# Performance work log

Hardware: AMD Instinct MI355X
Metric: run time of the kernel (lower is better)

## Reference

```python
import jax, jax.numpy as jnp
import numpy as np

C = 256
INTER = C // 8  # 32

def setup_inputs() -> dict:
    key = jax.random.key(0)
    ks = jax.random.split(key, 7)
    B, H, W = 8, 64, 64
    x = jax.random.normal(ks[0], (B, C, H, W), dtype=jnp.float32)
    # 1x1 convs == per-pixel linear maps
    Wq = jax.random.normal(ks[1], (INTER, C), dtype=jnp.float32) * (1.0 / np.sqrt(C))
    bq = jnp.zeros((INTER,), dtype=jnp.float32)
    Wk = jax.random.normal(ks[2], (INTER, C), dtype=jnp.float32) * (1.0 / np.sqrt(C))
    bk = jnp.zeros((INTER,), dtype=jnp.float32)
    Wv = jax.random.normal(ks[3], (C, C), dtype=jnp.float32) * (1.0 / np.sqrt(C))
    bv = jnp.zeros((C,), dtype=jnp.float32)
    gamma = jnp.asarray([0.1], dtype=jnp.float32)  # nonzero so attention path matters
    return {"x": x, "Wq": Wq, "bq": bq, "Wk": Wk, "bk": bk, "Wv": Wv, "bv": bv, "gamma": gamma}

def reference(x, Wq, bq, Wk, bk, Wv, bv, gamma):
    B, Cc, H, W = x.shape
    N = H * W
    xf = x.reshape(B, Cc, N)  # [B, C, N]
    # 1x1 conv projections (per-pixel linear)
    q = jnp.einsum('ic,bcn->bni', Wq, xf) + bq[None, None, :]   # [B, N, inter]
    k = jnp.einsum('ic,bcn->bin', Wk, xf) + bk[None, :, None]   # [B, inter, N]
    v = jnp.einsum('oc,bcn->bon', Wv, xf) + bv[None, :, None]   # [B, C, N]
    energy = jnp.einsum('bni,bim->bnm', q, k)                   # [B, N, N], unscaled
    attn = jax.nn.softmax(energy, axis=-1)                      # softmax over keys
    # out[b,c,i] = sum_j v[b,c,j] * attn[b,i,j]
    out = jnp.einsum('bcj,bij->bci', v, attn).reshape(B, Cc, H, W)
    return gamma[0] * out + x
```

## Files before the change

kernel.cpp:

```cpp
#include <hip/hip_runtime.h>
#include <hip/hip_bf16.h>

#define CCH 256
#define NPIX 4096
#define NB 8
#define LOG2E 1.4426950408889634f

typedef __attribute__((ext_vector_type(8))) short bf16x8;
typedef __attribute__((ext_vector_type(16))) float f32x16;

typedef __attribute__((address_space(3))) unsigned lds_u32;
typedef const __attribute__((address_space(1))) unsigned glb_u32;
#define GL_LDS16(gp, lp) \
    __builtin_amdgcn_global_load_lds((glb_u32*)(gp), (lds_u32*)(lp), 16, 0, 0)

static __device__ __forceinline__ unsigned pkbf(float a, float b) {
    union { __hip_bfloat16 h[2]; unsigned u; } p;
    p.h[0] = __float2bfloat16(a);
    p.h[1] = __float2bfloat16(b);
    return p.u;
}
static __device__ __forceinline__ unsigned short bf1(float a) {
    union { __hip_bfloat16 h; unsigned short s; } p;
    p.h = __float2bfloat16(a);
    return p.s;
}

__global__ void packw_kernel(const float* __restrict__ Wq,
                             const float* __restrict__ Wk,
                             const float* __restrict__ Wv,
                             unsigned short* __restrict__ Wb) {
    int i4 = blockIdx.x * 256 + threadIdx.x;
    if (i4 >= 20480) return;
    int e = i4 * 4;
    const float* src;
    if (e < 8192)       src = Wq + e;
    else if (e < 16384) src = Wk + (e - 8192);
    else                src = Wv + (e - 16384);
    float4 v = *(const float4*)src;
    uint2 o;
    o.x = pkbf(v.x, v.y);
    o.y = pkbf(v.z, v.w);
    *(uint2*)(Wb + e) = o;
}

__global__ __launch_bounds__(320) void qkv_kernel(
    const float* __restrict__ x,
    const unsigned short* __restrict__ Wb,
    const float* __restrict__ bq, const float* __restrict__ bk,
    const float* __restrict__ bv,
    unsigned short* __restrict__ q, unsigned short* __restrict__ k,
    unsigned short* __restrict__ v)
{
    __shared__ __align__(16) unsigned xp[128][36];

    const int t   = threadIdx.x;
    const int b   = blockIdx.x >> 7;
    const int px0 = (blockIdx.x & 127) * 32;

    const float4* gx = (const float4*)x + ((size_t)b * CCH * NPIX + px0) / 4;
    for (int i = t; i < 1024; i += 320) {
        int kp = i >> 3, p4 = i & 7;
        float4 lo = gx[(size_t)(2 * kp) * (NPIX / 4) + p4];
        float4 hi = gx[(size_t)(2 * kp + 1) * (NPIX / 4) + p4];
        uint4 pk4;
        pk4.x = pkbf(lo.x, hi.x);
        pk4.y = pkbf(lo.y, hi.y);
        pk4.z = pkbf(lo.z, hi.z);
        pk4.w = pkbf(lo.w, hi.w);
        *(uint4*)&xp[kp][p4 * 4] = pk4;
    }
    __syncthreads();

    const int w  = t >> 6;
    const int lane = t & 63;
    const int qi = lane & 31, h = lane >> 5;

    f32x16 acc[2];
    #pragma unroll
    for (int rt = 0; rt < 2; ++rt)
        #pragma unroll
        for (int r = 0; r < 16; ++r) acc[rt][r] = 0.f;

    #pragma unroll 4
    for (int ks = 0; ks < 16; ++ks) {
        union { unsigned uw[4]; bf16x8 v8; } xb;
        #pragma unroll
        for (int j = 0; j < 4; ++j) xb.uw[j] = xp[ks * 8 + 4 * h + j][qi];
        #pragma unroll
        for (int rt = 0; rt < 2; ++rt) {
            int row = (2 * w + rt) * 32 + qi;
            bf16x8 af = *(const bf16x8*)(Wb + (size_t)row * 256 + ks * 16 + h * 8);
            acc[rt] = __builtin_amdgcn_mfma_f32_32x32x16_bf16(af, xb.v8, acc[rt], 0, 0, 0);
        }
    }

    const int px = px0 + qi;
    const int pxv = px0 + ((qi & 19) | ((qi & 4) << 1) | ((qi & 8) >> 1));
    #pragma unroll
    for (int rt = 0; rt < 2; ++rt) {
        int tile = 2 * w + rt;
        if (tile < 2) {
            const float* bias = (tile == 0) ? bq : bk;
            unsigned short* outp = (tile == 0) ? q : k;
            float scale = (tile == 0) ? LOG2E : 1.0f;
            #pragma unroll
            for (int rg = 0; rg < 4; ++rg) {
                float vv[4];
                #pragma unroll
                for (int j = 0; j < 4; ++j) {
                    int outd = j + 8 * rg + 4 * h;
                    vv[j] = (acc[rt][4 * rg + j] + bias[outd]) * scale;
                }
                uint2 st;
                st.x = pkbf(vv[0], vv[1]);
                st.y = pkbf(vv[2], vv[3]);
                *(uint2*)(outp + ((size_t)b * NPIX + px) * 32 + 8 * rg + 4 * h) = st;
            }
        } else {
            #pragma unroll
            for (int r = 0; r < 16; ++r) {
                int outd = (r & 3) + 8 * (r >> 2) + 4 * h;
                int grow = (tile - 2) * 32 + outd;
                v[((size_t)b * CCH + grow) * NPIX + pxv] = bf1(acc[rt][r] + bv[grow]);
            }
        }
    }
}

__global__ __launch_bounds__(256, 2) void attn_kernel(
    const unsigned short* __restrict__ qg,
    const unsigned short* __restrict__ kg,
    const unsigned short* __restrict__ vg,
    const float* __restrict__ x,
    const float* __restrict__ gamma,
    float* __restrict__ out)
{
    __shared__ __align__(16) unsigned short Kl[3][64][4][8];
    __shared__ __align__(16) unsigned short Vl[3][128][8][8];

    const int t    = threadIdx.x;
    const int b    = blockIdx.x & 7;
    const int nc   = blockIdx.x >> 3;
    const int chh  = nc & 1;
    const int n0   = (nc >> 1) * 128;
    const int w    = t >> 6;
    const int lane = t & 63;
    const int qi = lane & 31, h = lane >> 5;

    bf16x8 qf0, qf1;
    {
        const unsigned short* qp = qg + ((size_t)b * NPIX + n0 + w * 32 + qi) * 32;
        qf0 = *(const bf16x8*)(qp + h * 8);
        qf1 = *(const bf16x8*)(qp + 16 + h * 8);
    }

    f32x16 acc[4];
    #pragma unroll
    for (int ct = 0; ct < 4; ++ct)
        #pragma unroll
        for (int r = 0; r < 16; ++r) acc[ct][r] = 0.f;
    float l_run = 0.f;

    const int srow = t >> 2;
    const unsigned short* kg_src =
        kg + ((size_t)b * NPIX + srow) * 32 + ((t & 3) ^ (srow & 3)) * 8;
    const int vrow = t >> 3;
    const unsigned short* vg_src =
        vg + ((size_t)b * CCH + chh * 128 + vrow) * NPIX + ((t & 7) ^ (vrow & 7)) * 8;
    char* kl_dst = (char*)Kl + t * 16;
    char* vl_dst = (char*)Vl + t * 16;

    const unsigned short* krd[2][2];
    #pragma unroll
    for (int sub = 0; sub < 2; ++sub)
        #pragma unroll
        for (int s = 0; s < 2; ++s)
            krd[sub][s] = &Kl[0][sub * 32 + qi][(2 * s + h) ^ (qi & 3)][0];
    const unsigned short* vrd[4];
    #pragma unroll
    for (int s = 0; s < 4; ++s)
        vrd[s] = &Vl[0][qi][(2 * s + h) ^ (qi & 7)][0];

    auto STAGE = [&](int buf, int kt) {
        const int k0 = kt * 64;
        GL_LDS16(kg_src + (size_t)k0 * 32, kl_dst + buf * 4096);
        #pragma unroll
        for (int p = 0; p < 4; ++p)
            GL_LDS16(vg_src + k0 + (size_t)p * 32 * NPIX,
                     vl_dst + buf * 16384 + p * 4096);
    };

    auto QKSM = [&](int kb, bf16x8* pf) {
        f32x16 s0, s1;
        #pragma unroll
        for (int r = 0; r < 16; ++r) { s0[r] = 0.f; s1[r] = 0.f; }
        s0 = __builtin_amdgcn_mfma_f32_32x32x16_bf16(*(const bf16x8*)(krd[0][0] + kb * 2048), qf0, s0, 0, 0, 0);
        s0 = __builtin_amdgcn_mfma_f32_32x32x16_bf16(*(const bf16x8*)(krd[0][1] + kb * 2048), qf1, s0, 0, 0, 0);
        s1 = __builtin_amdgcn_mfma_f32_32x32x16_bf16(*(const bf16x8*)(krd[1][0] + kb * 2048), qf0, s1, 0, 0, 0);
        s1 = __builtin_amdgcn_mfma_f32_32x32x16_bf16(*(const bf16x8*)(krd[1][1] + kb * 2048), qf1, s1, 0, 0, 0);
        #pragma unroll
        for (int sub = 0; sub < 2; ++sub) {
            const f32x16& sv = sub ? s1 : s0;
            #pragma unroll
            for (int sp = 0; sp < 2; ++sp) {
                union { unsigned uw[4]; bf16x8 v8; } pk;
                float ps = 0.f;
                #pragma unroll
                for (int c = 0; c < 4; ++c) {
                    float ea = exp2f(sv[8 * sp + 2 * c]);
                    float eb = exp2f(sv[8 * sp + 2 * c + 1]);
                    ps += ea + eb;
                    pk.uw[c] = pkbf(ea, eb);
                }
                l_run += ps;
                pf[2 * sub + sp] = pk.v8;
            }
        }
    };

    auto PV = [&](int vb, const bf16x8* pf) {
        __builtin_amdgcn_s_setprio(1);
        #pragma unroll
        for (int ct = 0; ct < 4; ++ct) {
            #pragma unroll
            for (int s = 0; s < 4; ++s) {
                bf16x8 vf = *(const bf16x8*)(vrd[s] + vb * 8192 + ct * 2048);
                acc[ct] = __builtin_amdgcn_mfma_f32_32x32x16_bf16(vf, pf[s], acc[ct], 0, 0, 0);
            }
        }
        __builtin_amdgcn_s_setprio(0);
    };

#define VMBAR(N) do { asm volatile("s_waitcnt vmcnt(" #N ")" ::: "memory"); \
                      __builtin_amdgcn_s_barrier(); } while (0)

    bf16x8 pfA[4], pfB[4], pfC[4];

    STAGE(0, 0);
    VMBAR(0);
    STAGE(1, 1);
    QKSM(0, pfA);
    VMBAR(4);

    #pragma unroll 1
    for (int m = 0; m < 20; ++m) {
        STAGE(2, 3 * m + 2); QKSM(1, pfB); PV(0, pfA); VMBAR(4);
        STAGE(0, 3 * m + 3); QKSM(2, pfC); PV(1, pfB); VMBAR(4);
        STAGE(1, 3 * m + 4); QKSM(0, pfA); PV(2, pfC); VMBAR(4);
    }
    STAGE(2, 62); QKSM(1, pfB); PV(0, pfA); VMBAR(4);
    STAGE(0, 63); QKSM(2, pfC); PV(1, pfB); VMBAR(4);
    QKSM(0, pfA); PV(2, pfC);
    VMBAR(0);
    PV(0, pfA);

    float l = l_run + __shfl_xor(l_run, 32, 64);
    const float rs = gamma[0] / l;
    #pragma unroll
    for (int ct = 0; ct < 4; ++ct) {
        #pragma unroll
        for (int r = 0; r < 16; ++r) {
            int c = chh * 128 + ct * 32 + (r & 3) + 8 * (r >> 2) + 4 * h;
            size_t off = ((size_t)b * CCH + c) * NPIX + n0 + w * 32 + qi;
            out[off] = rs * acc[ct][r] + x[off];
        }
    }
#undef VMBAR
}

extern "C" void kernel_launch(void* const* d_in, const int* in_sizes, int n_in,
                              void* d_out, int out_size, void* d_ws, size_t ws_size,
                              hipStream_t stream) {
    const float* x     = (const float*)d_in[0];
    const float* Wq    = (const float*)d_in[1];
    const float* bq    = (const float*)d_in[2];
    const float* Wk    = (const float*)d_in[3];
    const float* bk    = (const float*)d_in[4];
    const float* Wv    = (const float*)d_in[5];
    const float* bv    = (const float*)d_in[6];
    const float* gamma = (const float*)d_in[7];
    float* out = (float*)d_out;

    unsigned short* Wb = (unsigned short*)d_ws;
    unsigned short* qw = Wb + 320 * 256;
    unsigned short* kw = qw + (size_t)NB * NPIX * 32;
    unsigned short* vw = kw + (size_t)NB * NPIX * 32;

    packw_kernel<<<dim3(80), dim3(256), 0, stream>>>(Wq, Wk, Wv, Wb);
    qkv_kernel<<<dim3(NB * (NPIX / 32)), dim3(320), 0, stream>>>(
        x, Wb, bq, bk, bv, qw, kw, vw);
    attn_kernel<<<dim3(512), dim3(256), 0, stream>>>(
        qw, kw, vw, x, gamma, out);
}
```

Measured before the change: 162.6 us.

## Warp-specialize attention: QK/softmax waves feed P via LDS to PV waves

Restructures the attention kernel into producer/consumer wave groups. Four waves compute QK^T and exp, writing bf16 probabilities to a double-buffered LDS tile. Four other waves stream V and run the PV MFMAs over all 256 channels. This removes the old duplication where QK/softmax was recomputed for each channel half, and it halves the grid to 256 blocks of 512 threads. The cost is a full barrier every key tile, extra LDS traffic for P, and lower occupancy.

```diff
diff --git a/kernel.cpp b/kernel.cpp
--- a/kernel.cpp
+++ b/kernel.cpp
@@ -13,6 +13,10 @@
 typedef const __attribute__((address_space(1))) unsigned glb_u32;
 #define GL_LDS16(gp, lp) \
     __builtin_amdgcn_global_load_lds((glb_u32*)(gp), (lds_u32*)(lp), 16, 0, 0)
+
+#define PBAR() do { __builtin_amdgcn_sched_barrier(0); \
+    asm volatile("s_waitcnt vmcnt(0) lgkmcnt(0)" ::: "memory"); \
+    __builtin_amdgcn_s_barrier(); __builtin_amdgcn_sched_barrier(0); } while (0)
 
 static __device__ __forceinline__ unsigned pkbf(float a, float b) {
     union { __hip_bfloat16 h[2]; unsigned u; } p;
@@ -128,7 +132,7 @@
     }
 }
 
-__global__ __launch_bounds__(256, 2) void attn_kernel(
+__global__ __launch_bounds__(512, 2) void attn_kernel(
     const unsigned short* __restrict__ qg,
     const unsigned short* __restrict__ kg,
     const unsigned short* __restrict__ vg,
@@ -136,137 +140,176 @@
     const float* __restrict__ gamma,
     float* __restrict__ out)
 {
-    __shared__ __align__(16) unsigned short Kl[3][64][4][8];
-    __shared__ __align__(16) unsigned short Vl[3][128][8][8];
+    __shared__ __align__(16) unsigned short Kl[2][64][4][8];
+    __shared__ __align__(16) unsigned short Vl[2][256][8][8];
+    __shared__ __align__(16) unsigned short Pt[2][128][72];
+    __shared__ float Lx[128];
 
     const int t    = threadIdx.x;
     const int b    = blockIdx.x & 7;
-    const int nc   = blockIdx.x >> 3;
-    const int chh  = nc & 1;
-    const int n0   = (nc >> 1) * 128;
+    const int n0   = (blockIdx.x >> 3) * 128;
     const int w    = t >> 6;
     const int lane = t & 63;
     const int qi = lane & 31, h = lane >> 5;
 
-    bf16x8 qf0, qf1;
-    {
-        const unsigned short* qp = qg + ((size_t)b * NPIX + n0 + w * 32 + qi) * 32;
-        qf0 = *(const bf16x8*)(qp + h * 8);
-        qf1 = *(const bf16x8*)(qp + 16 + h * 8);
+    if (w < 4) {
+        const int qt = w;
+        bf16x8 qf0, qf1;
+        {
+            const unsigned short* qp = qg + ((size_t)b * NPIX + n0 + qt * 32 + qi) * 32;
+            qf0 = *(const bf16x8*)(qp + h * 8);
+            qf1 = *(const bf16x8*)(qp + 16 + h * 8);
+        }
+        const int srow = t >> 2;
+        const unsigned short* kg_src =
+            kg + ((size_t)b * NPIX + srow) * 32 + ((t & 3) ^ (srow & 3)) * 8;
+        char* kl_dst = (char*)Kl + t * 16;
+        const unsigned short* krd[2][2];
+        #pragma unroll
+        for (int sub = 0; sub < 2; ++sub)
+            #pragma unroll
+            for (int s = 0; s < 2; ++s)
+                krd[sub][s] = &Kl[0][sub * 32 + qi][(2 * s + h) ^ (qi & 3)][0];
+        unsigned short* pw_base = &Pt[0][32 * qt + qi][4 * h];
+
+        float l_run = 0.f;
+
+        auto STAGEK = [&](int buf, int kt) {
+            GL_LDS16(kg_src + (size_t)kt * 2048, kl_dst + buf * 4096);
+        };
+        auto QKSM = [&](int kt) {
+            const int kb = kt & 1;
+            f32x16 s0, s1;
+            #pragma unroll
+            for (int r = 0; r < 16; ++r) { s0[r] = 0.f; s1[r] = 0.f; }
+            s0 = __builtin_amdgcn_mfma_f32_32x32x16_bf16(*(const bf16x8*)(krd[0][0] + kb * 2048), qf0, s0, 0, 0, 0);
+            s0 = __builtin_amdgcn_mfma_f32_32x32x16_bf16(*(const bf16x8*)(krd[0][1] + kb * 2048), qf1, s0, 0, 0, 0);
+            s1 = __builtin_amdgcn_mfma_f32_32x32x16_bf16(*(const bf16x8*)(krd[1][0] + kb * 2048), qf0, s1, 0, 0, 0);
+            s1 = __builtin_amdgcn_mfma_f32_32x32x16_bf16(*(const bf16x8*)(krd[1][1] + kb * 2048), qf1, s1, 0, 0, 0);
+            unsigned short* pw = pw_base + (kt & 1) * 9216;
+            #pragma unroll
+            for (int sb = 0; sb < 2; ++sb) {
+                const f32x16& sv = sb ? s1 : s0;
+                #pragma unroll
+                for (int m = 0; m < 4; ++m) {
+                    float e0 = exp2f(sv[4 * m + 0]);
+                    float e1 = exp2f(sv[4 * m + 1]);
+                    float e2 = exp2f(sv[4 * m + 2]);
+                    float e3 = exp2f(sv[4 * m + 3]);
+                    l_run += (e0 + e1) + (e2 + e3);
+                    uint2 val;
+                    val.x = pkbf(e0, e1);
+                    val.y = pkbf(e2, e3);
+                    *(uint2*)(pw + 32 * sb + 8 * m) = val;
+                }
+            }
+        };
+
+        STAGEK(0, 0);
+        PBAR();
+        QKSM(0);
+        STAGEK(1, 1);
+        PBAR();
+        #pragma unroll 1
+        for (int tt = 0; tt < 64; ++tt) {
+            if (tt < 63) {
+                QKSM(tt + 1);
+                if (tt < 62) STAGEK(tt & 1, tt + 2);
+            } else {
+                float lt = l_run + __shfl_xor(l_run, 32, 64);
+                if (lane < 32) Lx[32 * qt + lane] = lt;
+            }
+            PBAR();
+        }
+    } else {
+        const int cw = w - 4;
+        const unsigned short* vg_src =
+            vg + ((size_t)b * CCH + 64 * cw + (lane >> 3)) * NPIX +
+            ((lane & 7) ^ ((lane >> 3) & 7)) * 8;
+        char* vl_dst = (char*)Vl + cw * 8192 + lane * 16;
+        const unsigned short* vrd[2][4];
+        #pragma unroll
+        for (int ct = 0; ct < 2; ++ct)
+            #pragma unroll
+            for (int s = 0; s < 4; ++s)
+                vrd[ct][s] = &Vl[0][64 * cw + 32 * ct + qi][(2 * s + h) ^ (qi & 7)][0];
+        const unsigned short* prd = &Pt[0][qi][4 * h];
+
+        f32x16 acc[2][4];
+        #pragma unroll
+        for (int ct = 0; ct < 2; ++ct)
+            #pragma unroll
+            for (int qt = 0; qt < 4; ++qt)
+                #pragma unroll
+                for (int r = 0; r < 16; ++r) acc[ct][qt][r] = 0.f;
+
+        auto STAGEV = [&](int buf, int kt) {
+            const unsigned short* s0 = vg_src + kt * 64;
+            char* d0 = vl_dst + buf * 32768;
+            #pragma unroll
+            for (int p = 0; p < 8; ++p)
+                GL_LDS16(s0 + (size_t)(8 * p) * NPIX, d0 + p * 1024);
+        };
+        auto PV = [&](int tt) {
+            const int vb = tt & 1;
+            bf16x8 vf[2][4];
+            #pragma unroll
+            for (int ct = 0; ct < 2; ++ct)
+                #pragma unroll
+                for (int s = 0; s < 4; ++s)
+                    vf[ct][s] = *(const bf16x8*)(vrd[ct][s] + vb * 16384);
+            const unsigned short* pr0 = prd + (tt & 1) * 9216;
+            __builtin_amdgcn_s_setprio(1);
+            #pragma unroll
+            for (int qt = 0; qt < 4; ++qt) {
+                bf16x8 pf[4];
+                #pragma unroll
+                for (int s = 0; s < 4; ++s) {
+                    const unsigned short* pr = pr0 + qt * 2304 + s * 16;
+                    uint2 lo = *(const uint2*)(pr);
+                    uint2 hi = *(const uint2*)(pr + 8);
+                    union { unsigned uw[4]; bf16x8 v8; } pk;
+                    pk.uw[0] = lo.x; pk.uw[1] = lo.y;
+                    pk.uw[2] = hi.x; pk.uw[3] = hi.y;
+                    pf[s] = pk.v8;
+                }
+                #pragma unroll
+                for (int ct = 0; ct < 2; ++ct)
+                    #pragma unroll
+                    for (int s = 0; s < 4; ++s)
+                        acc[ct][qt] = __builtin_amdgcn_mfma_f32_32x32x16_bf16(
+                            vf[ct][s], pf[s], acc[ct][qt], 0, 0, 0);
+            }
+            __builtin_amdgcn_s_setprio(0);
+        };
+
+        STAGEV(0, 0);
+        PBAR();
+        PBAR();
+        #pragma unroll 1
+        for (int tt = 0; tt < 64; ++tt) {
+            if (tt < 63) STAGEV((tt + 1) & 1, tt + 1);
+            PV(tt);
+            PBAR();
+        }
+
+        const float g = gamma[0];
+        float rsl[4];
+        #pragma unroll
+        for (int qt = 0; qt < 4; ++qt) rsl[qt] = g / Lx[32 * qt + qi];
+        #pragma unroll
+        for (int ct = 0; ct < 2; ++ct) {
+            #pragma unroll
+            for (int qt = 0; qt < 4; ++qt) {
+                #pragma unroll
+                for (int r = 0; r < 16; ++r) {
+                    int c = 64 * cw + 32 * ct + (r & 3) + 8 * (r >> 2) + 4 * h;
+                    size_t off = ((size_t)b * CCH + c) * NPIX + n0 + 32 * qt + qi;
+                    out[off] = rsl[qt] * acc[ct][qt][r] + x[off];
+                }
+            }
+        }
     }
-
-    f32x16 acc[4];
-    #pragma unroll
-    for (int ct = 0; ct < 4; ++ct)
-        #pragma unroll
-        for (int r = 0; r < 16; ++r) acc[ct][r] = 0.f;
-    float l_run = 0.f;
-
-    const int srow = t >> 2;
-    const unsigned short* kg_src =
-        kg + ((size_t)b * NPIX + srow) * 32 + ((t & 3) ^ (srow & 3)) * 8;
-    const int vrow = t >> 3;
-    const unsigned short* vg_src =
-        vg + ((size_t)b * CCH + chh * 128 + vrow) * NPIX + ((t & 7) ^ (vrow & 7)) * 8;
-    char* kl_dst = (char*)Kl + t * 16;
-    char* vl_dst = (char*)Vl + t * 16;
-
-    const unsigned short* krd[2][2];
-    #pragma unroll
-    for (int sub = 0; sub < 2; ++sub)
-        #pragma unroll
-        for (int s = 0; s < 2; ++s)
-            krd[sub][s] = &Kl[0][sub * 32 + qi][(2 * s + h) ^ (qi & 3)][0];
-    const unsigned short* vrd[4];
-    #pragma unroll
-    for (int s = 0; s < 4; ++s)
-        vrd[s] = &Vl[0][qi][(2 * s + h) ^ (qi & 7)][0];
-
-    auto STAGE = [&](int buf, int kt) {
-        const int k0 = kt * 64;
-        GL_LDS16(kg_src + (size_t)k0 * 32, kl_dst + buf * 4096);
-        #pragma unroll
-        for (int p = 0; p < 4; ++p)
-            GL_LDS16(vg_src + k0 + (size_t)p * 32 * NPIX,
-                     vl_dst + buf * 16384 + p * 4096);
-    };
-
-    auto QKSM = [&](int kb, bf16x8* pf) {
-        f32x16 s0, s1;
-        #pragma unroll
-        for (int r = 0; r < 16; ++r) { s0[r] = 0.f; s1[r] = 0.f; }
-        s0 = __builtin_amdgcn_mfma_f32_32x32x16_bf16(*(const bf16x8*)(krd[0][0] + kb * 2048), qf0, s0, 0, 0, 0);
-        s0 = __builtin_amdgcn_mfma_f32_32x32x16_bf16(*(const bf16x8*)(krd[0][1] + kb * 2048), qf1, s0, 0, 0, 0);
-        s1 = __builtin_amdgcn_mfma_f32_32x32x16_bf16(*(const bf16x8*)(krd[1][0] + kb * 2048), qf0, s1, 0, 0, 0);
-        s1 = __builtin_amdgcn_mfma_f32_32x32x16_bf16(*(const bf16x8*)(krd[1][1] + kb * 2048), qf1, s1, 0, 0, 0);
-        #pragma unroll
-        for (int sub = 0; sub < 2; ++sub) {
-            const f32x16& sv = sub ? s1 : s0;
-            #pragma unroll
-            for (int sp = 0; sp < 2; ++sp) {
-                union { unsigned uw[4]; bf16x8 v8; } pk;
-                float ps = 0.f;
-                #pragma unroll
-                for (int c = 0; c < 4; ++c) {
-                    float ea = exp2f(sv[8 * sp + 2 * c]);
-                    float eb = exp2f(sv[8 * sp + 2 * c + 1]);
-                    ps += ea + eb;
-                    pk.uw[c] = pkbf(ea, eb);
-                }
-                l_run += ps;
-                pf[2 * sub + sp] = pk.v8;
-            }
-        }
-    };
-
-    auto PV = [&](int vb, const bf16x8* pf) {
-        __builtin_amdgcn_s_setprio(1);
-        #pragma unroll
-        for (int ct = 0; ct < 4; ++ct) {
-            #pragma unroll
-            for (int s = 0; s < 4; ++s) {
-                bf16x8 vf = *(const bf16x8*)(vrd[s] + vb * 8192 + ct * 2048);
-                acc[ct] = __builtin_amdgcn_mfma_f32_32x32x16_bf16(vf, pf[s], acc[ct], 0, 0, 0);
-            }
-        }
-        __builtin_amdgcn_s_setprio(0);
-    };
-
-#define VMBAR(N) do { asm volatile("s_waitcnt vmcnt(" #N ")" ::: "memory"); \
-                      __builtin_amdgcn_s_barrier(); } while (0)
-
-    bf16x8 pfA[4], pfB[4], pfC[4];
-
-    STAGE(0, 0);
-    VMBAR(0);
-    STAGE(1, 1);
-    QKSM(0, pfA);
-    VMBAR(4);
-
-    #pragma unroll 1
-    for (int m = 0; m < 20; ++m) {
-        STAGE(2, 3 * m + 2); QKSM(1, pfB); PV(0, pfA); VMBAR(4);
-        STAGE(0, 3 * m + 3); QKSM(2, pfC); PV(1, pfB); VMBAR(4);
-        STAGE(1, 3 * m + 4); QKSM(0, pfA); PV(2, pfC); VMBAR(4);
-    }
-    STAGE(2, 62); QKSM(1, pfB); PV(0, pfA); VMBAR(4);
-    STAGE(0, 63); QKSM(2, pfC); PV(1, pfB); VMBAR(4);
-    QKSM(0, pfA); PV(2, pfC);
-    VMBAR(0);
-    PV(0, pfA);
-
-    float l = l_run + __shfl_xor(l_run, 32, 64);
-    const float rs = gamma[0] / l;
-    #pragma unroll
-    for (int ct = 0; ct < 4; ++ct) {
-        #pragma unroll
-        for (int r = 0; r < 16; ++r) {
-            int c = chh * 128 + ct * 32 + (r & 3) + 8 * (r >> 2) + 4 * h;
-            size_t off = ((size_t)b * CCH + c) * NPIX + n0 + w * 32 + qi;
-            out[off] = rs * acc[ct][r] + x[off];
-        }
-    }
-#undef VMBAR
 }
 
 extern "C" void kernel_launch(void* const* d_in, const int* in_sizes, int n_in,
@@ -290,6 +333,6 @@
     packw_kernel<<<dim3(80), dim3(256), 0, stream>>>(Wq, Wk, Wv, Wb);
     qkv_kernel<<<dim3(NB * (NPIX / 32)), dim3(320), 0, stream>>>(
         x, Wb, bq, bk, bv, qw, kw, vw);
-    attn_kernel<<<dim3(512), dim3(256), 0, stream>>>(
+    attn_kernel<<<dim3(256), dim3(512), 0, stream>>>(
         qw, kw, vw, x, gamma, out);
 }
```

After: 143.0 us. -12.1%, faster.

## Compute all 256 channels per block to halve QK/softmax recompute, double-buffer pipeline

Applied to the files above, without the earlier changes.

Each attention block now covers all 256 value channels for its 128 queries instead of splitting channels across two blocks. This halves the grid and removes the duplicated QK^T and exp work that each channel half used to redo. The three-stage software pipeline (QK of the next tile overlapping PV of the current one) is replaced by a simple double-buffered loop with a full vmcnt/lgkmcnt barrier each iteration. In exchange there are twice as many accumulator registers (8 f32x16 per thread), a larger LDS footprint, only 256 blocks, and less overlap between loads and compute.

```diff
diff --git a/kernel.cpp b/kernel.cpp
--- a/kernel.cpp
+++ b/kernel.cpp
@@ -13,6 +13,10 @@
 typedef const __attribute__((address_space(1))) unsigned glb_u32;
 #define GL_LDS16(gp, lp) \
     __builtin_amdgcn_global_load_lds((glb_u32*)(gp), (lds_u32*)(lp), 16, 0, 0)
+
+#define TBAR() do { __builtin_amdgcn_sched_barrier(0); \
+    asm volatile("s_waitcnt vmcnt(0) lgkmcnt(0)" ::: "memory"); \
+    __builtin_amdgcn_s_barrier(); __builtin_amdgcn_sched_barrier(0); } while (0)
 
 static __device__ __forceinline__ unsigned pkbf(float a, float b) {
     union { __hip_bfloat16 h[2]; unsigned u; } p;
@@ -136,14 +140,12 @@
     const float* __restrict__ gamma,
     float* __restrict__ out)
 {
-    __shared__ __align__(16) unsigned short Kl[3][64][4][8];
-    __shared__ __align__(16) unsigned short Vl[3][128][8][8];
+    __shared__ __align__(16) unsigned short Kl[2][64][4][8];
+    __shared__ __align__(16) unsigned short Vl[2][256][8][8];
 
     const int t    = threadIdx.x;
     const int b    = blockIdx.x & 7;
-    const int nc   = blockIdx.x >> 3;
-    const int chh  = nc & 1;
-    const int n0   = (nc >> 1) * 128;
+    const int n0   = (blockIdx.x >> 3) * 128;
     const int w    = t >> 6;
     const int lane = t & 63;
     const int qi = lane & 31, h = lane >> 5;
@@ -155,19 +157,12 @@
         qf1 = *(const bf16x8*)(qp + 16 + h * 8);
     }
 
-    f32x16 acc[4];
-    #pragma unroll
-    for (int ct = 0; ct < 4; ++ct)
-        #pragma unroll
-        for (int r = 0; r < 16; ++r) acc[ct][r] = 0.f;
-    float l_run = 0.f;
-
     const int srow = t >> 2;
     const unsigned short* kg_src =
         kg + ((size_t)b * NPIX + srow) * 32 + ((t & 3) ^ (srow & 3)) * 8;
     const int vrow = t >> 3;
     const unsigned short* vg_src =
-        vg + ((size_t)b * CCH + chh * 128 + vrow) * NPIX + ((t & 7) ^ (vrow & 7)) * 8;
+        vg + ((size_t)b * CCH + vrow) * NPIX + ((t & 7) ^ (vrow & 7)) * 8;
     char* kl_dst = (char*)Kl + t * 16;
     char* vl_dst = (char*)Vl + t * 16;
 
@@ -182,23 +177,40 @@
     for (int s = 0; s < 4; ++s)
         vrd[s] = &Vl[0][qi][(2 * s + h) ^ (qi & 7)][0];
 
-    auto STAGE = [&](int buf, int kt) {
-        const int k0 = kt * 64;
-        GL_LDS16(kg_src + (size_t)k0 * 32, kl_dst + buf * 4096);
-        #pragma unroll
-        for (int p = 0; p < 4; ++p)
-            GL_LDS16(vg_src + k0 + (size_t)p * 32 * NPIX,
-                     vl_dst + buf * 16384 + p * 4096);
+    f32x16 acc[8];
+    #pragma unroll
+    for (int ct = 0; ct < 8; ++ct)
+        #pragma unroll
+        for (int r = 0; r < 16; ++r) acc[ct][r] = 0.f;
+    float l_run = 0.f;
+
+    auto STAGE = [&](int kt) {
+        const int buf = kt & 1;
+        GL_LDS16(kg_src + (size_t)kt * 2048, kl_dst + buf * 4096);
+        const unsigned short* s0 = vg_src + kt * 64;
+        char* d0 = vl_dst + buf * 32768;
+        #pragma unroll
+        for (int p = 0; p < 8; ++p)
+            GL_LDS16(s0 + (size_t)(32 * p) * NPIX, d0 + p * 4096);
     };
 
-    auto QKSM = [&](int kb, bf16x8* pf) {
+    STAGE(0);
+    TBAR();
+
+    #pragma unroll 1
+    for (int tt = 0; tt < 64; ++tt) {
+        if (tt < 63) STAGE(tt + 1);
+
+        const int kb = (tt & 1) * 2048;
         f32x16 s0, s1;
         #pragma unroll
         for (int r = 0; r < 16; ++r) { s0[r] = 0.f; s1[r] = 0.f; }
-        s0 = __builtin_amdgcn_mfma_f32_32x32x16_bf16(*(const bf16x8*)(krd[0][0] + kb * 2048), qf0, s0, 0, 0, 0);
-        s0 = __builtin_amdgcn_mfma_f32_32x32x16_bf16(*(const bf16x8*)(krd[0][1] + kb * 2048), qf1, s0, 0, 0, 0);
-        s1 = __builtin_amdgcn_mfma_f32_32x32x16_bf16(*(const bf16x8*)(krd[1][0] + kb * 2048), qf0, s1, 0, 0, 0);
-        s1 = __builtin_amdgcn_mfma_f32_32x32x16_bf16(*(const bf16x8*)(krd[1][1] + kb * 2048), qf1, s1, 0, 0, 0);
+        s0 = __builtin_amdgcn_mfma_f32_32x32x16_bf16(*(const bf16x8*)(krd[0][0] + kb), qf0, s0, 0, 0, 0);
+        s0 = __builtin_amdgcn_mfma_f32_32x32x16_bf16(*(const bf16x8*)(krd[0][1] + kb), qf1, s0, 0, 0, 0);
+        s1 = __builtin_amdgcn_mfma_f32_32x32x16_bf16(*(const bf16x8*)(krd[1][0] + kb), qf0, s1, 0, 0, 0);
+        s1 = __builtin_amdgcn_mfma_f32_32x32x16_bf16(*(const bf16x8*)(krd[1][1] + kb), qf1, s1, 0, 0, 0);
+
+        bf16x8 pf[4];
         #pragma unroll
         for (int sub = 0; sub < 2; ++sub) {
             const f32x16& sv = sub ? s1 : s0;
@@ -217,56 +229,33 @@
                 pf[2 * sub + sp] = pk.v8;
             }
         }
-    };
-
-    auto PV = [&](int vb, const bf16x8* pf) {
+
+        const int vb = (tt & 1) * 16384;
         __builtin_amdgcn_s_setprio(1);
         #pragma unroll
-        for (int ct = 0; ct < 4; ++ct) {
+        for (int ct = 0; ct < 8; ++ct) {
             #pragma unroll
             for (int s = 0; s < 4; ++s) {
-                bf16x8 vf = *(const bf16x8*)(vrd[s] + vb * 8192 + ct * 2048);
+                bf16x8 vf = *(const bf16x8*)(vrd[s] + vb + ct * 2048);
                 acc[ct] = __builtin_amdgcn_mfma_f32_32x32x16_bf16(vf, pf[s], acc[ct], 0, 0, 0);
             }
         }
         __builtin_amdgcn_s_setprio(0);
-    };
-
-#define VMBAR(N) do { asm volatile("s_waitcnt vmcnt(" #N ")" ::: "memory"); \
-                      __builtin_amdgcn_s_barrier(); } while (0)
-
-    bf16x8 pfA[4], pfB[4], pfC[4];
-
-    STAGE(0, 0);
-    VMBAR(0);
-    STAGE(1, 1);
-    QKSM(0, pfA);
-    VMBAR(4);
-
-    #pragma unroll 1
-    for (int m = 0; m < 20; ++m) {
-        STAGE(2, 3 * m + 2); QKSM(1, pfB); PV(0, pfA); VMBAR(4);
-        STAGE(0, 3 * m + 3); QKSM(2, pfC); PV(1, pfB); VMBAR(4);
-        STAGE(1, 3 * m + 4); QKSM(0, pfA); PV(2, pfC); VMBAR(4);
-    }
-    STAGE(2, 62); QKSM(1, pfB); PV(0, pfA); VMBAR(4);
-    STAGE(0, 63); QKSM(2, pfC); PV(1, pfB); VMBAR(4);
-    QKSM(0, pfA); PV(2, pfC);
-    VMBAR(0);
-    PV(0, pfA);
+
+        TBAR();
+    }
 
     float l = l_run + __shfl_xor(l_run, 32, 64);
     const float rs = gamma[0] / l;
     #pragma unroll
-    for (int ct = 0; ct < 4; ++ct) {
+    for (int ct = 0; ct < 8; ++ct) {
         #pragma unroll
         for (int r = 0; r < 16; ++r) {
-            int c = chh * 128 + ct * 32 + (r & 3) + 8 * (r >> 2) + 4 * h;
+            int c = ct * 32 + (r & 3) + 8 * (r >> 2) + 4 * h;
             size_t off = ((size_t)b * CCH + c) * NPIX + n0 + w * 32 + qi;
             out[off] = rs * acc[ct][r] + x[off];
         }
     }
-#undef VMBAR
 }
 
 extern "C" void kernel_launch(void* const* d_in, const int* in_sizes, int n_in,
@@ -290,6 +279,6 @@
     packw_kernel<<<dim3(80), dim3(256), 0, stream>>>(Wq, Wk, Wv, Wb);
     qkv_kernel<<<dim3(NB * (NPIX / 32)), dim3(320), 0, stream>>>(
         x, Wb, bq, bk, bv, qw, kw, vw);
-    attn_kernel<<<dim3(512), dim3(256), 0, stream>>>(
+    attn_kernel<<<dim3(256), dim3(256), 0, stream>>>(
         qw, kw, vw, x, gamma, out);
 }
```

Measured after the change: 176.1 us. +8.3%, slower.
